# Performance work log

Measured on AMD Instinct MI355X. Metric: run time of the kernel, lower is better.

The kernel has to match this reference:

```python
import jax, jax.numpy as jnp
import numpy as np

N = 50000
E = 1_600_000
NODE_DIM = 64
EDGE_DIM = 32
HIDDEN = 64


def setup_inputs() -> dict:
    key = jax.random.key(0)
    ks = jax.random.split(key, 7)
    x = jax.random.normal(ks[0], (N, NODE_DIM), dtype=jnp.float32)
    edge_index = jax.random.randint(ks[1], (2, E), 0, N, dtype=jnp.int64)
    edge_attr = jax.random.normal(ks[2], (E, EDGE_DIM), dtype=jnp.float32)
    in_dim = NODE_DIM + EDGE_DIM
    W1 = jax.random.normal(ks[3], (in_dim, HIDDEN), dtype=jnp.float32) / np.sqrt(in_dim)
    b1 = jnp.zeros((HIDDEN,), dtype=jnp.float32)
    W2 = jax.random.normal(ks[4], (HIDDEN, NODE_DIM), dtype=jnp.float32) / np.sqrt(HIDDEN)
    b2 = jnp.zeros((NODE_DIM,), dtype=jnp.float32)
    return {"x": x, "edge_index": edge_index, "edge_attr": edge_attr,
            "W1": W1, "b1": b1, "W2": W2, "b2": b2}


def reference(x, edge_index, edge_attr, W1, b1, W2, b2):
    # PyG flow source_to_target: x_i = target node features = x[edge_index[1]]
    dst = edge_index[1]
    x_i = x[dst]                                      # [E, NODE_DIM] gather
    msg_in = jnp.concatenate([x_i, edge_attr], -1)    # [E, NODE_DIM+EDGE_DIM]
    h = jax.nn.relu(msg_in @ W1 + b1)                 # [E, HIDDEN] (dropout = identity at inference)
    m = jax.nn.relu(h @ W2 + b2)                      # [E, NODE_DIM]
    n = x.shape[0]
    summed = jax.ops.segment_sum(m, dst, num_segments=n)                 # [N, NODE_DIM]
    cnt = jax.ops.segment_sum(jnp.ones((m.shape[0],), m.dtype), dst, num_segments=n)
    aggr = summed / jnp.maximum(cnt, 1.0)[:, None]    # scatter-mean (0 for isolated nodes)
    return aggr + x                                   # residual (Identity since dims match)
```

## Files before the change

### kernel.cpp

```cpp
#include <hip/hip_runtime.h>

#define NODES 50000
#define NEDGE 1600000
#define ND 64
#define ED 32
#define HID 64
#define IN_DIM 96

#define TW 16
#define H_LD   72
#define MT_LD  24
#define W1_LD  104
#define W2_LD  72
#define SC_ELEM 1536

typedef __bf16 bf16_t;
typedef __bf16 bf16x4_t __attribute__((ext_vector_type(4)));
typedef __bf16 bf16x8_t __attribute__((ext_vector_type(8)));
typedef float  f32x4_t  __attribute__((ext_vector_type(4)));
typedef unsigned int u32;

#define SCAN_B 256
#define SCAN_NBLK ((NODES + SCAN_B - 1) / SCAN_B)

#define NXCD 8
#define NODES_PER_G ((NODES + NXCD - 1) / NXCD)

__global__ void zero_kernel(float* __restrict__ out, int* __restrict__ cnt) {
    int i = blockIdx.x * blockDim.x + threadIdx.x;
    int stride = gridDim.x * blockDim.x;
    const int total = NODES * ND;
    for (int idx = i; idx < total; idx += stride) out[idx] = 0.0f;
    for (int idx = i; idx < NODES; idx += stride) cnt[idx] = 0;
}

__global__ void hist_kernel(const int* __restrict__ ei, int* __restrict__ cnt,
                            int* __restrict__ rank) {
    int i = blockIdx.x * blockDim.x + threadIdx.x;
    int stride = gridDim.x * blockDim.x;
    for (int e = i; e < NEDGE; e += stride)
        rank[e] = atomicAdd(&cnt[ei[NEDGE + e]], 1);
}

__global__ void scan_sum_kernel(const int* __restrict__ cnt, int* __restrict__ bsum) {
    __shared__ int sh[SCAN_B];
    const int t = threadIdx.x, b = blockIdx.x;
    const int i = b * SCAN_B + t;
    sh[t] = (i < NODES) ? cnt[i] : 0;
    __syncthreads();
    for (int d = SCAN_B / 2; d > 0; d >>= 1) {
        if (t < d) sh[t] += sh[t + d];
        __syncthreads();
    }
    if (t == 0) bsum[b] = sh[0];
}

__global__ void scan_top_kernel(int* __restrict__ bsum) {
    __shared__ int sh[SCAN_B];
    const int t = threadIdx.x;
    sh[t] = (t < SCAN_NBLK) ? bsum[t] : 0;
    __syncthreads();
    for (int d = 1; d < SCAN_B; d <<= 1) {
        int v = (t >= d) ? sh[t - d] : 0;
        __syncthreads();
        sh[t] += v;
        __syncthreads();
    }
    if (t < SCAN_NBLK) bsum[t] = (t == 0) ? 0 : sh[t - 1];
}

__global__ void scan_fill_kernel(const int* __restrict__ cnt, const int* __restrict__ bsum,
                                 int* __restrict__ cursor) {
    __shared__ int sh[SCAN_B];
    const int t = threadIdx.x, b = blockIdx.x;
    const int i = b * SCAN_B + t;
    int v = (i < NODES) ? cnt[i] : 0;
    sh[t] = v;
    __syncthreads();
    for (int d = 1; d < SCAN_B; d <<= 1) {
        int u = (t >= d) ? sh[t - d] : 0;
        __syncthreads();
        sh[t] += u;
        __syncthreads();
    }
    if (i < NODES) cursor[i] = bsum[b] + sh[t] - v;
}

__global__ void bucket_kernel(const int* __restrict__ ei, const int* __restrict__ cursor,
                              const int* __restrict__ rank, int2* __restrict__ pd) {
    const int g   = blockIdx.x & (NXCD - 1);
    const int bg  = blockIdx.x >> 3;
    const int bpg = gridDim.x >> 3;
    const int lo  = g * NODES_PER_G;
    const int hi  = min(lo + NODES_PER_G, NODES);
    int i = bg * blockDim.x + threadIdx.x;
    int stride = bpg * blockDim.x;
    for (int e = i; e < NEDGE; e += stride) {
        int d = ei[NEDGE + e];
        if (d >= lo && d < hi)
            pd[cursor[d] + rank[e]] = make_int2(e, d);
    }
}

static __device__ __forceinline__ uint2 packbf(float4 v) {
    bf16x4_t p = {(bf16_t)v.x, (bf16_t)v.y, (bf16_t)v.z, (bf16_t)v.w};
    union { bf16x4_t b; uint2 u; } c;
    c.b = p;
    return c.u;
}

__global__ __launch_bounds__(256, 4)
void edge_mlp_mfma(const float* __restrict__ x,
                   const float* __restrict__ edge_attr,
                   const float* __restrict__ W1, const float* __restrict__ b1,
                   const float* __restrict__ W2, const float* __restrict__ b2,
                   const int2* __restrict__ pd,
                   float* __restrict__ out_sum)
{
    __shared__ __align__(16) bf16_t w1T[HID * W1_LD];
    __shared__ __align__(16) bf16_t w2T[ND * W2_LD];
    __shared__ __align__(16) bf16_t sc_all[4 * SC_ELEM];

    const int t    = threadIdx.x;
    const int lane = t & 63;
    const int w    = t >> 6;
    const int col  = lane & 15;
    const int kq   = lane >> 4;
    const int e    = lane >> 2;
    const int c    = lane & 3;

    bf16_t* hS = sc_all + w * SC_ELEM;
    bf16_t* mT = hS;

    for (int i = t; i < IN_DIM * HID / 4; i += 256) {
        float4 v = ((const float4*)W1)[i];
        int k = i >> 4, j4 = (i & 15) * 4;
        w1T[(j4 + 0) * W1_LD + k] = (bf16_t)v.x;
        w1T[(j4 + 1) * W1_LD + k] = (bf16_t)v.y;
        w1T[(j4 + 2) * W1_LD + k] = (bf16_t)v.z;
        w1T[(j4 + 3) * W1_LD + k] = (bf16_t)v.w;
    }
    for (int i = t; i < HID * ND / 4; i += 256) {
        float4 v = ((const float4*)W2)[i];
        int k = i >> 4, j4 = (i & 15) * 4;
        w2T[(j4 + 0) * W2_LD + k] = (bf16_t)v.x;
        w2T[(j4 + 1) * W2_LD + k] = (bf16_t)v.y;
        w2T[(j4 + 2) * W2_LD + k] = (bf16_t)v.z;
        w2T[(j4 + 3) * W2_LD + k] = (bf16_t)v.w;
    }
    float b1r[4], b2r[4];
    #pragma unroll
    for (int nt = 0; nt < 4; ++nt) {
        b1r[nt] = b1[col + 16 * nt];
        b2r[nt] = b2[col + 16 * nt];
    }
    __syncthreads();

    const int ntiles = NEDGE / TW;
    const int wid = blockIdx.x * 4 + w;
    const int nw  = gridDim.x * 4;

    float4 xv0, xv1, xv2, xv3;
    float4 ev0, ev1;
    int    dstv;

    {
        const int eb0 = wid * TW;
        int2 rec = pd[eb0 + e];
        dstv = pd[eb0 + col].y;
        const float4* xr = (const float4*)(x + (size_t)rec.y * ND);
        const float4* er = (const float4*)(edge_attr + (size_t)rec.x * ED);
        xv0 = xr[2 * c]; xv1 = xr[2 * c + 1]; xv2 = xr[8 + 2 * c]; xv3 = xr[8 + 2 * c + 1];
        ev0 = er[2 * c]; ev1 = er[2 * c + 1];
    }

    for (int tile = wid; tile < ntiles; tile += nw) {
        const int dcur = dstv;

        uint2 x0p = packbf(xv0), x1p = packbf(xv1), x2p = packbf(xv2), x3p = packbf(xv3);
        uint2 e0p = packbf(ev0), e1p = packbf(ev1);

        if (tile + nw < ntiles) {
            const int eb1 = (tile + nw) * TW;
            int2 rec = pd[eb1 + e];
            dstv = pd[eb1 + col].y;
            const float4* xr = (const float4*)(x + (size_t)rec.y * ND);
            const float4* er = (const float4*)(edge_attr + (size_t)rec.x * ED);
            xv0 = xr[2 * c]; xv1 = xr[2 * c + 1]; xv2 = xr[8 + 2 * c]; xv3 = xr[8 + 2 * c + 1];
            ev0 = er[2 * c]; ev1 = er[2 * c + 1];
        }

        const int sl = col * 4 + kq;
        union U8 { u32 u[4]; bf16x8_t v; } a0, a1, a2;
        a0.u[0] = __shfl((int)x0p.x, sl, 64); a0.u[1] = __shfl((int)x0p.y, sl, 64);
        a0.u[2] = __shfl((int)x1p.x, sl, 64); a0.u[3] = __shfl((int)x1p.y, sl, 64);
        a1.u[0] = __shfl((int)x2p.x, sl, 64); a1.u[1] = __shfl((int)x2p.y, sl, 64);
        a1.u[2] = __shfl((int)x3p.x, sl, 64); a1.u[3] = __shfl((int)x3p.y, sl, 64);
        a2.u[0] = __shfl((int)e0p.x, sl, 64); a2.u[1] = __shfl((int)e0p.y, sl, 64);
        a2.u[2] = __shfl((int)e1p.x, sl, 64); a2.u[3] = __shfl((int)e1p.y, sl, 64);

        f32x4_t acc[4];
        #pragma unroll
        for (int nt = 0; nt < 4; ++nt) {
            const bf16_t* wrow = &w1T[(col + 16 * nt) * W1_LD + kq * 8];
            bf16x8_t f0 = *(const bf16x8_t*)(wrow + 0 * 32);
            bf16x8_t f1 = *(const bf16x8_t*)(wrow + 1 * 32);
            bf16x8_t f2 = *(const bf16x8_t*)(wrow + 2 * 32);
            acc[nt] = (f32x4_t){0.0f, 0.0f, 0.0f, 0.0f};
            acc[nt] = __builtin_amdgcn_mfma_f32_16x16x32_bf16(a0.v, f0, acc[nt], 0, 0, 0);
            acc[nt] = __builtin_amdgcn_mfma_f32_16x16x32_bf16(a1.v, f1, acc[nt], 0, 0, 0);
            acc[nt] = __builtin_amdgcn_mfma_f32_16x16x32_bf16(a2.v, f2, acc[nt], 0, 0, 0);
        }
        #pragma unroll
        for (int nt = 0; nt < 4; ++nt)
            #pragma unroll
            for (int r = 0; r < 4; ++r)
                hS[(4 * kq + r) * H_LD + col + 16 * nt] =
                    (bf16_t)fmaxf(acc[nt][r] + b1r[nt], 0.0f);

        const int hb = col * H_LD + kq * 8;
        bf16x8_t ah0 = *(const bf16x8_t*)&hS[hb + 0 * 32];
        bf16x8_t ah1 = *(const bf16x8_t*)&hS[hb + 1 * 32];
        f32x4_t acc2[4];
        #pragma unroll
        for (int nt = 0; nt < 4; ++nt) {
            const bf16_t* wrow = &w2T[(col + 16 * nt) * W2_LD + kq * 8];
            bf16x8_t f0 = *(const bf16x8_t*)(wrow + 0 * 32);
            bf16x8_t f1 = *(const bf16x8_t*)(wrow + 1 * 32);
            acc2[nt] = (f32x4_t){0.0f, 0.0f, 0.0f, 0.0f};
            acc2[nt] = __builtin_amdgcn_mfma_f32_16x16x32_bf16(ah0, f0, acc2[nt], 0, 0, 0);
            acc2[nt] = __builtin_amdgcn_mfma_f32_16x16x32_bf16(ah1, f1, acc2[nt], 0, 0, 0);
        }

        const int dA = __builtin_amdgcn_readlane(dcur, 0);
        const int dB = __builtin_amdgcn_readlane(dcur, 15);
        if (dA == dB) {
            float s0 = 0.0f, s1 = 0.0f, s2 = 0.0f, s3 = 0.0f;
            #pragma unroll
            for (int r = 0; r < 4; ++r) {
                s0 += fmaxf(acc2[0][r] + b2r[0], 0.0f);
                s1 += fmaxf(acc2[1][r] + b2r[1], 0.0f);
                s2 += fmaxf(acc2[2][r] + b2r[2], 0.0f);
                s3 += fmaxf(acc2[3][r] + b2r[3], 0.0f);
            }
            s0 += __shfl_xor(s0, 16); s0 += __shfl_xor(s0, 32);
            s1 += __shfl_xor(s1, 16); s1 += __shfl_xor(s1, 32);
            s2 += __shfl_xor(s2, 16); s2 += __shfl_xor(s2, 32);
            s3 += __shfl_xor(s3, 16); s3 += __shfl_xor(s3, 32);
            const float sv = (kq == 0) ? s0 : (kq == 1) ? s1 : (kq == 2) ? s2 : s3;
            atomicAdd(&out_sum[(size_t)dA * ND + lane], sv);
        } else {
            #pragma unroll
            for (int nt = 0; nt < 4; ++nt)
                #pragma unroll
                for (int r = 0; r < 4; ++r)
                    mT[(col + 16 * nt) * MT_LD + 4 * kq + r] =
                        (bf16_t)fmaxf(acc2[nt][r] + b2r[nt], 0.0f);

            bf16x8_t v0 = *(const bf16x8_t*)&mT[lane * MT_LD + 0];
            bf16x8_t v1 = *(const bf16x8_t*)&mT[lane * MT_LD + 8];
            float mval[16];
            #pragma unroll
            for (int j = 0; j < 8; ++j) { mval[j] = (float)v0[j]; mval[8 + j] = (float)v1[j]; }

            int cur = dA;
            float s = 0.0f;
            #pragma unroll
            for (int r = 0; r < TW; ++r) {
                const int d = __builtin_amdgcn_readlane(dcur, r);
                if (d != cur) {
                    atomicAdd(&out_sum[(size_t)cur * ND + lane], s);
                    s = 0.0f; cur = d;
                }
                s += mval[r];
            }
            atomicAdd(&out_sum[(size_t)cur * ND + lane], s);
        }
    }
}

__global__ void finalize_kernel(const float* __restrict__ x,
                                const int* __restrict__ cnt,
                                float* __restrict__ out)
{
    int i = blockIdx.x * blockDim.x + threadIdx.x;
    int stride = gridDim.x * blockDim.x;
    const int total4 = NODES * ND / 4;
    for (int idx = i; idx < total4; idx += stride) {
        const int n = idx / (ND / 4);
        const float inv = 1.0f / fmaxf((float)cnt[n], 1.0f);
        float4 s = ((const float4*)out)[idx];
        float4 xv = ((const float4*)x)[idx];
        float4 r;
        r.x = s.x * inv + xv.x;
        r.y = s.y * inv + xv.y;
        r.z = s.z * inv + xv.z;
        r.w = s.w * inv + xv.w;
        ((float4*)out)[idx] = r;
    }
}

extern "C" void kernel_launch(void* const* d_in, const int* in_sizes, int n_in,
                              void* d_out, int out_size, void* d_ws, size_t ws_size,
                              hipStream_t stream) {
    const float* x  = (const float*)d_in[0];
    const int*   ei = (const int*)d_in[1];
    const float* ea = (const float*)d_in[2];
    const float* W1 = (const float*)d_in[3];
    const float* b1 = (const float*)d_in[4];
    const float* W2 = (const float*)d_in[5];
    const float* b2 = (const float*)d_in[6];
    float* out = (float*)d_out;

    int*  cnt    = (int*)d_ws;
    int*  cursor = cnt + NODES;
    int2* pd     = (int2*)(cursor + NODES);
    int*  bsum   = (int*)(pd + NEDGE);
    int*  rank   = bsum + 256;

    hipLaunchKernelGGL(zero_kernel, dim3(2048), dim3(256), 0, stream, out, cnt);
    hipLaunchKernelGGL(hist_kernel, dim3(2048), dim3(256), 0, stream, ei, cnt, rank);
    hipLaunchKernelGGL(scan_sum_kernel, dim3(SCAN_NBLK), dim3(SCAN_B), 0, stream, cnt, bsum);
    hipLaunchKernelGGL(scan_top_kernel, dim3(1), dim3(SCAN_B), 0, stream, bsum);
    hipLaunchKernelGGL(scan_fill_kernel, dim3(SCAN_NBLK), dim3(SCAN_B), 0, stream, cnt, bsum, cursor);
    hipLaunchKernelGGL(bucket_kernel, dim3(2048), dim3(256), 0, stream, ei, cursor, rank, pd);
    hipLaunchKernelGGL(edge_mlp_mfma, dim3(1024), dim3(256), 0, stream,
                       x, ea, W1, b1, W2, b2, pd, out);
    hipLaunchKernelGGL(finalize_kernel, dim3(1600), dim3(256), 0, stream, x, cnt, out);
}
```

Baseline: 189.2 us.

## Pack dst and rank into one word and partition MLP tiles per XCD

The histogram kernel now stores each edge's destination and its rank within that destination as a single 32-bit word (dst in the high 16 bits, rank in the low 16). The bucket kernel, which each of the 8 XCD groups runs over all edges, then reads one 4-byte word per edge instead of both edge_index and rank. The edge MLP kernel also gives each XCD a contiguous range of tiles in dst-sorted order, so x gathers and output atomics for nearby nodes stay in that XCD's L2. The packing relies on node ids and per-node degree fitting in 16 bits, and the locality benefit relies on blocks being dispatched round-robin across XCDs.

```diff
diff --git a/kernel.cpp b/kernel.cpp
--- a/kernel.cpp
+++ b/kernel.cpp
@@ -35,11 +35,14 @@
 }
 
 __global__ void hist_kernel(const int* __restrict__ ei, int* __restrict__ cnt,
-                            int* __restrict__ rank) {
+                            u32* __restrict__ pk) {
     int i = blockIdx.x * blockDim.x + threadIdx.x;
     int stride = gridDim.x * blockDim.x;
-    for (int e = i; e < NEDGE; e += stride)
-        rank[e] = atomicAdd(&cnt[ei[NEDGE + e]], 1);
+    for (int e = i; e < NEDGE; e += stride) {
+        int d = ei[NEDGE + e];
+        int r = atomicAdd(&cnt[d], 1);
+        pk[e] = ((u32)d << 16) | (u32)r;
+    }
 }
 
 __global__ void scan_sum_kernel(const int* __restrict__ cnt, int* __restrict__ bsum) {
@@ -86,8 +89,8 @@
     if (i < NODES) cursor[i] = bsum[b] + sh[t] - v;
 }
 
-__global__ void bucket_kernel(const int* __restrict__ ei, const int* __restrict__ cursor,
-                              const int* __restrict__ rank, int2* __restrict__ pd) {
+__global__ void bucket_kernel(const u32* __restrict__ pk, const int* __restrict__ cursor,
+                              int2* __restrict__ pd) {
     const int g   = blockIdx.x & (NXCD - 1);
     const int bg  = blockIdx.x >> 3;
     const int bpg = gridDim.x >> 3;
@@ -96,9 +99,10 @@
     int i = bg * blockDim.x + threadIdx.x;
     int stride = bpg * blockDim.x;
     for (int e = i; e < NEDGE; e += stride) {
-        int d = ei[NEDGE + e];
+        u32 p = pk[e];
+        int d = (int)(p >> 16);
         if (d >= lo && d < hi)
-            pd[cursor[d] + rank[e]] = make_int2(e, d);
+            pd[cursor[d] + (int)(p & 0xffffu)] = make_int2(e, d);
     }
 }
 
@@ -157,15 +161,20 @@
     __syncthreads();
 
     const int ntiles = NEDGE / TW;
-    const int wid = blockIdx.x * 4 + w;
-    const int nw  = gridDim.x * 4;
+    const int tpx    = ntiles / NXCD;
+    const int xg     = blockIdx.x & (NXCD - 1);
+    const int bg     = blockIdx.x >> 3;
+    const int base   = xg * tpx;
+    const int lim    = base + tpx;
+    const int wix    = bg * 4 + w;
+    const int nwx    = (gridDim.x >> 3) * 4;
 
     float4 xv0, xv1, xv2, xv3;
     float4 ev0, ev1;
     int    dstv;
 
     {
-        const int eb0 = wid * TW;
+        const int eb0 = (base + wix) * TW;
         int2 rec = pd[eb0 + e];
         dstv = pd[eb0 + col].y;
         const float4* xr = (const float4*)(x + (size_t)rec.y * ND);
@@ -174,14 +183,14 @@
         ev0 = er[2 * c]; ev1 = er[2 * c + 1];
     }
 
-    for (int tile = wid; tile < ntiles; tile += nw) {
+    for (int tile = base + wix; tile < lim; tile += nwx) {
         const int dcur = dstv;
 
         uint2 x0p = packbf(xv0), x1p = packbf(xv1), x2p = packbf(xv2), x3p = packbf(xv3);
         uint2 e0p = packbf(ev0), e1p = packbf(ev1);
 
-        if (tile + nw < ntiles) {
-            const int eb1 = (tile + nw) * TW;
+        if (tile + nwx < lim) {
+            const int eb1 = (tile + nwx) * TW;
             int2 rec = pd[eb1 + e];
             dstv = pd[eb1 + col].y;
             const float4* xr = (const float4*)(x + (size_t)rec.y * ND);
@@ -316,14 +325,14 @@
     int*  cursor = cnt + NODES;
     int2* pd     = (int2*)(cursor + NODES);
     int*  bsum   = (int*)(pd + NEDGE);
-    int*  rank   = bsum + 256;
+    u32*  pk     = (u32*)(bsum + 256);
 
     hipLaunchKernelGGL(zero_kernel, dim3(2048), dim3(256), 0, stream, out, cnt);
-    hipLaunchKernelGGL(hist_kernel, dim3(2048), dim3(256), 0, stream, ei, cnt, rank);
+    hipLaunchKernelGGL(hist_kernel, dim3(2048), dim3(256), 0, stream, ei, cnt, pk);
     hipLaunchKernelGGL(scan_sum_kernel, dim3(SCAN_NBLK), dim3(SCAN_B), 0, stream, cnt, bsum);
     hipLaunchKernelGGL(scan_top_kernel, dim3(1), dim3(SCAN_B), 0, stream, bsum);
     hipLaunchKernelGGL(scan_fill_kernel, dim3(SCAN_NBLK), dim3(SCAN_B), 0, stream, cnt, bsum, cursor);
-    hipLaunchKernelGGL(bucket_kernel, dim3(2048), dim3(256), 0, stream, ei, cursor, rank, pd);
+    hipLaunchKernelGGL(bucket_kernel, dim3(2048), dim3(256), 0, stream, pk, cursor, pd);
     hipLaunchKernelGGL(edge_mlp_mfma, dim3(1024), dim3(256), 0, stream,
                        x, ea, W1, b1, W2, b2, pd, out);
     hipLaunchKernelGGL(finalize_kernel, dim3(1600), dim3(256), 0, stream, x, cnt, out);
```

Result: faster. 184.8 us (median of 2 runs) (-2.3%).
